# Performance work log

Hardware: AMD Instinct MI355X
Metric: run time of the kernel (lower is better)

The kernel has to match this reference:

```python
import jax, jax.numpy as jnp
import numpy as np

C = 512
H_HEADS = 8  # self-attn heads (num_heads) and cross-attn heads (n_heads), both 8


def _self_attn(x, Wq, Wkv):
    # x: [B,N,C]; shared (ModuleParallel) linear weights, qkv_bias=False
    B, N, _ = x.shape
    h, d = H_HEADS, C // H_HEADS
    q = (x @ Wq.T).reshape(B, N, h, d).transpose(0, 2, 1, 3)          # [B,h,N,d]
    kv = (x @ Wkv.T).reshape(B, N, 2, h, d).transpose(2, 0, 3, 1, 4)  # [2,B,h,N,d]
    k, v = kv[0], kv[1]
    attn = jax.nn.softmax(jnp.einsum('bhnd,bhmd->bhnm', q, k) * (d ** -0.5), axis=-1)
    y = jnp.einsum('bhnm,bhmd->bhnd', attn, v).transpose(0, 2, 1, 3).reshape(B, N, C)
    return y


def _judger(y_self, y_other, Wj1, bj1, Wj2, bj2):
    # Mlp_2(2C->C->C) with exact GELU, then softmax over channel dim
    hdn = jax.nn.gelu(jnp.concatenate([y_self, y_other], axis=-1) @ Wj1.T + bj1, approximate=False)
    return jax.nn.softmax(hdn @ Wj2.T + bj2, axis=-1)


def _cross_attn(yq, ykv, kn_row, vn_row, Win, bin_, Wout, bout, rel):
    # Vectorized form of the per-sample loop: each token is a seq-len-1 query
    # attending over 2 keys: [noise_k + yq, yq * relation_score].
    B, N, _ = yq.shape
    h, d = H_HEADS, C // H_HEADS
    qw, kw, vw = Win[:C], Win[C:2 * C], Win[2 * C:]
    bq, bk, bv = bin_[:C], bin_[C:2 * C], bin_[2 * C:]
    k_in = jnp.stack([kn_row + yq, yq * rel], axis=-2)   # [B,N,2,C]
    v_in = jnp.stack([vn_row + yq, ykv], axis=-2)        # [B,N,2,C]
    qp = (yq @ qw.T + bq).reshape(B, N, h, d)
    kp = (k_in @ kw.T + bk).reshape(B, N, 2, h, d)
    vp = (v_in @ vw.T + bv).reshape(B, N, 2, h, d)
    scores = jnp.einsum('bnhd,bnkhd->bnhk', qp, kp) * (d ** -0.5)
    w = jax.nn.softmax(scores, axis=-1)
    o = jnp.einsum('bnhk,bnkhd->bnhd', w, vp).reshape(B, N, C)
    return o @ Wout.T + bout


def setup_inputs() -> dict:
    key = jax.random.key(0)
    ks = jax.random.split(key, 16)
    B, N = 8, 1024
    s = 0.02
    inp = {
        'x0': jax.random.normal(ks[0], (B, N, C), jnp.float32),
        'x1': jax.random.normal(ks[1], (B, N, C), jnp.float32),
        'H': 32, 'W': 32,
        'Wq': jax.random.normal(ks[2], (C, C), jnp.float32) * s,
        'Wkv': jax.random.normal(ks[3], (2 * C, C), jnp.float32) * s,
        'Wj1': jax.random.normal(ks[4], (C, 2 * C), jnp.float32) * s,
        'bj1': jnp.zeros((C,), jnp.float32),
        'Wj2': jax.random.normal(ks[5], (C, C), jnp.float32) * s,
        'bj2': jnp.zeros((C,), jnp.float32),
        'kn': jax.random.normal(ks[6], (2, C), jnp.float32),
        'vn': jax.random.normal(ks[7], (2, C), jnp.float32),
        'Wc0_in': jax.random.normal(ks[8], (3 * C, C), jnp.float32) * s,
        'bc0_in': jnp.zeros((3 * C,), jnp.float32),
        'Wc0_out': jax.random.normal(ks[9], (C, C), jnp.float32) * s,
        'bc0_out': jnp.zeros((C,), jnp.float32),
        'Wc1_in': jax.random.normal(ks[10], (3 * C, C), jnp.float32) * s,
        'bc1_in': jnp.zeros((3 * C,), jnp.float32),
        'Wc1_out': jax.random.normal(ks[11], (C, C), jnp.float32) * s,
        'bc1_out': jnp.zeros((C,), jnp.float32),
        'Wp': jax.random.normal(ks[12], (C, C), jnp.float32) * s,
        'bp': jnp.zeros((C,), jnp.float32),
    }
    return inp


def reference(x0, x1, H, W, Wq, Wkv, Wj1, bj1, Wj2, bj2, kn, vn,
              Wc0_in, bc0_in, Wc0_out, bc0_out, Wc1_in, bc1_in, Wc1_out, bc1_out,
              Wp, bp):
    # Dual self-attention (shared q/kv projections across modalities, sr_ratio=1)
    y0 = _self_attn(x0, Wq, Wkv)
    y1 = _self_attn(x1, Wq, Wkv)
    # Noise-augmented relation-gated cross-attention (vectorized over batch)
    rel0 = _judger(y0, y1, Wj1, bj1, Wj2, bj2)
    rel1 = _judger(y1, y0, Wj1, bj1, Wj2, bj2)
    new0 = y0 + _cross_attn(y0, y1, kn[0], vn[0], Wc0_in, bc0_in, Wc0_out, bc0_out, rel0)
    new1 = y1 + _cross_attn(y1, y0, kn[1], vn[1], Wc1_in, bc1_in, Wc1_out, bc1_out, rel1)
    out0 = new0 @ Wp.T + bp
    out1 = new1 @ Wp.T + bp
    return jnp.stack([out0, out1])  # [2,B,N,C]
```

## Files before the change

kernel.cpp:

```cpp
#include <hip/hip_runtime.h>

typedef unsigned short u16;
typedef u16 u16x8 __attribute__((ext_vector_type(8)));
typedef __bf16 bf16x8 __attribute__((ext_vector_type(8)));
typedef __bf16 bf16x2 __attribute__((ext_vector_type(2)));
typedef float f32x4 __attribute__((ext_vector_type(4)));

__device__ __forceinline__ float b2f(u16 h) {
  union { unsigned u; float f; } x; x.u = ((unsigned)h) << 16; return x.f;
}
__device__ __forceinline__ u16 f2b(float f) {
  union { float f; unsigned u; } x; x.f = f;
  unsigned r = x.u + 0x7FFFu + ((x.u >> 16) & 1u);
  return (u16)(r >> 16);
}
__device__ __forceinline__ f32x4 mfma16(bf16x8 a, bf16x8 b, f32x4 c) {
  return __builtin_amdgcn_mfma_f32_16x16x32_bf16(a, b, c, 0, 0, 0);
}
__device__ __forceinline__ void gload16(const void* g, void* l) {
  __builtin_amdgcn_global_load_lds(
      (const __attribute__((address_space(1))) void*)g,
      (__attribute__((address_space(3))) void*)l, 16, 0, 0);
}
#define WAITV4 asm volatile("s_waitcnt vmcnt(4)" ::: "memory")
#define WAITV0 asm volatile("s_waitcnt vmcnt(0)" ::: "memory")
#define WAITL0 asm volatile("s_waitcnt lgkmcnt(0)" ::: "memory")
#define BARRIER asm volatile("s_barrier" ::: "memory")

__global__ __launch_bounds__(256) void xcvt_k(const float* __restrict__ x0,
                                              const float* __restrict__ x1,
                                              u16* __restrict__ out) {
  int b = blockIdx.x;
  const float* src = (b < 4096) ? x0 : x1;
  u16* dst = out + (b < 4096 ? 0 : 4194304);
  int i = (b & 4095) * 1024 + threadIdx.x * 4;
  float4 v = *(const float4*)&src[i];
  dst[i + 0] = f2b(v.x); dst[i + 1] = f2b(v.y);
  dst[i + 2] = f2b(v.z); dst[i + 3] = f2b(v.w);
}

__global__ __launch_bounds__(256) void wcvt_k(
    const float* __restrict__ wq, const float* __restrict__ wkv,
    const float* __restrict__ wj1, const float* __restrict__ wj2,
    const float* __restrict__ wci0, const float* __restrict__ wci1,
    const float* __restrict__ wp, u16* __restrict__ wsb) {
  int b = blockIdx.x; const float* src; size_t doff; int lb;
  if      (b < 256)  { src = wq;   doff = 0;       lb = b; }
  else if (b < 768)  { src = wkv;  doff = 262144;  lb = b - 256; }
  else if (b < 1280) { src = wj1;  doff = 786432;  lb = b - 768; }
  else if (b < 1536) { src = wj2;  doff = 1310720; lb = b - 1280; }
  else if (b < 2304) { src = wci0; doff = 1572864; lb = b - 1536; }
  else if (b < 3072) { src = wci1; doff = 2359296; lb = b - 2304; }
  else               { src = wp;   doff = 3145728; lb = b - 3072; }
  int i = lb * 1024 + threadIdx.x * 4;
  float4 v = *(const float4*)&src[i];
  u16* dst = wsb + doff + i;
  u16 c0 = f2b(v.x), c1 = f2b(v.y), c2 = f2b(v.z), c3 = f2b(v.w);
  dst[0] = c0; dst[1] = c1; dst[2] = c2; dst[3] = c3;
  if (b >= 3072) {
    int row = i >> 9, col = i & 511;
    u16* f0 = wsb + 3932160 + (size_t)row * 1024 + col;
    u16* f1 = wsb + 4456448 + (size_t)row * 1024 + col;
    f0[0] = c0; f0[1] = c1; f0[2] = c2; f0[3] = c3;
    f1[0] = c0; f1[1] = c1; f1[2] = c2; f1[3] = c3;
  }
}

__global__ __launch_bounds__(256) void tcvt_k(const float* __restrict__ w0,
                                              const float* __restrict__ w1,
                                              u16* __restrict__ o0,
                                              u16* __restrict__ o1) {
  __shared__ u16 t[64][65];
  const int b = blockIdx.x;
  const float* src = (b & 64) ? w1 : w0;
  u16* dst = (b & 64) ? o1 : o0;
  const int r0 = ((b >> 3) & 7) * 64, c0 = (b & 7) * 64;
  const int tid = threadIdx.x;
#pragma unroll
  for (int i = 0; i < 16; i++) {
    int idx = tid + i * 256;
    int r = idx >> 6, c = idx & 63;
    t[r][c] = f2b(src[(size_t)(r0 + r) * 512 + c0 + c]);
  }
  __syncthreads();
#pragma unroll
  for (int i = 0; i < 16; i++) {
    int idx = tid + i * 256;
    int c = idx >> 6, r = idx & 63;
    dst[(size_t)(c0 + c) * 512 + r0 + r] = t[r][c];
  }
}

__global__ __launch_bounds__(256) void cvec_k(
    const float* __restrict__ kn, const float* __restrict__ vn,
    const float* __restrict__ bp, const float* __restrict__ bco0,
    const float* __restrict__ bco1, const u16* __restrict__ wci0,
    const u16* __restrict__ wci1, const u16* __restrict__ wp,
    float* __restrict__ out) {
  int idx = blockIdx.x * 256 + threadIdx.x;
  int which = idx >> 9, col = idx & 511;
  const float* src; const u16* w; float acc;
  if (which < 4) {
    int s = which & 1, isv = which >> 1;
    src = (isv ? vn : kn) + s * 512;
    w = (s ? wci1 : wci0) + (isv ? 524288 : 262144) + (size_t)col * 512;
    acc = 0.f;
  } else {
    int s = which & 1;
    src = s ? bco1 : bco0;
    w = wp + (size_t)col * 512;
    acc = bp[col];
  }
  for (int k = 0; k < 512; k += 8) {
    u16x8 w8 = *(const u16x8*)&w[k];
#pragma unroll
    for (int j = 0; j < 8; j++) acc += src[k + j] * b2f(w8[j]);
  }
  out[idx] = acc;
}

template<int EPI, int AMODE>
__global__ __launch_bounds__(512, 4) void gemm9_k(
    const u16* __restrict__ A, int astr, int K1, int K,
    const u16* __restrict__ W0, const u16* __restrict__ W1,
    const float* __restrict__ b0, const float* __restrict__ b1,
    void* __restrict__ outp, int ostr, int ncol) {
  __shared__ u16 SM[32768];
  const int tid = threadIdx.x;
  const int lane = tid & 63;
  const int wv = tid >> 6;
  const int wr = wv >> 1, wc = wv & 1;
  const int lr = lane & 15, lg = lane >> 4;
  const int L = blockIdx.x;
  const int nrow = gridDim.x / ncol;
  int row_b, col_b;
  if ((nrow & 7) == 0) {
    int xcd = L & 7, s = L >> 3;
    row_b = xcd * (nrow >> 3) + s / ncol;
    col_b = s % ncol;
  } else { row_b = L % nrow; col_b = L / nrow; }
  const int row0 = row_b * 128, col0 = col_b * 128;
  const int strm = (row0 >= 8192) ? 1 : 0;
  const u16* W = strm ? W1 : W0;
  const float* bias = strm ? b1 : b0;
  const int shift = (AMODE == 4 && col0 >= 1536) ? 512 : 0;
  const int cxor  = (AMODE == 4 && col0 >= 1536) ? 8192 : 0;
  const int rL = tid >> 3;
  const int bcl = (lane & 7) * 16;

  f32x4 acc[2][4];
#pragma unroll
  for (int m = 0; m < 2; m++)
#pragma unroll
    for (int n = 0; n < 4; n++) acc[m][n] = f32x4{0.f, 0.f, 0.f, 0.f};

  const int nk = K >> 6;

  auto stage = [&](int k0, int buf) {
    const int Ab = buf * 16384, Wb = buf * 16384 + 8192;
#pragma unroll
    for (int ch = 0; ch < 2; ch++) {
      int r = ch * 64 + rL;
      int bcs = bcl ^ ((r & 7) << 4);
      const char* asrc;
      if constexpr (AMODE == 3) {
        if (k0 < K1)
          asrc = (const char*)(A + (size_t)(row0 + r) * astr) + k0 * 2 + bcs;
        else
          asrc = (const char*)(A + (size_t)((row0 + r) ^ 8192) * astr) +
                 (k0 - K1) * 2 + bcs;
      } else {
        asrc = (const char*)(A + (size_t)((row0 + r) ^ cxor) * astr) +
               k0 * 2 + bcs;
      }
      gload16(asrc, &SM[Ab + (ch * 64 + wv * 8) * 64]);
      const char* wsrc =
          (const char*)(W + (size_t)(col0 - shift + r) * K) + k0 * 2 + bcs;
      gload16(wsrc, &SM[Wb + (ch * 64 + wv * 8) * 64]);
    }
  };

  stage(0, 0);
  for (int t = 0; t < nk; t++) {
    const int buf = t & 1;
    if (t + 1 < nk) {
      stage((t + 1) * 64, buf ^ 1);
      WAITV4;
    } else {
      WAITV0;
    }
    BARRIER;
    const int Ab = buf * 16384, Wb = buf * 16384 + 8192;
#pragma unroll
    for (int kk = 0; kk < 2; kk++) {
      const int c = kk * 32 + lg * 8;
      bf16x8 af[2], wf[4];
#pragma unroll
      for (int m = 0; m < 2; m++) {
        int r = wr * 32 + m * 16 + lr;
        af[m] = *(const bf16x8*)&SM[Ab + r * 64 + (c ^ ((r & 7) << 3))];
      }
#pragma unroll
      for (int n = 0; n < 4; n++) {
        int r = wc * 64 + n * 16 + lr;
        wf[n] = *(const bf16x8*)&SM[Wb + r * 64 + (c ^ ((r & 7) << 3))];
      }
#pragma unroll
      for (int m = 0; m < 2; m++)
#pragma unroll
        for (int n = 0; n < 4; n++)
          acc[m][n] = mfma16(af[m], wf[n], acc[m][n]);
    }
    WAITL0;
    BARRIER;
  }

#pragma unroll
  for (int m = 0; m < 2; m++)
#pragma unroll
    for (int n = 0; n < 4; n++)
#pragma unroll
      for (int r = 0; r < 4; r++) {
        int grow = row0 + wr * 32 + m * 16 + lg * 4 + r;
        int gcol = col0 + wc * 64 + n * 16 + lr;
        float v = acc[m][n][r];
        if (bias) v += bias[gcol - shift];
        if (EPI == 1) v = 0.5f * v * (1.0f + erff(v * 0.70710678118f));
        if (EPI == 3) ((float*)outp)[(size_t)grow * ostr + gcol] = v;
        else          ((u16*)outp)[(size_t)grow * ostr + gcol] = f2b(v);
      }
}

__global__ __launch_bounds__(256) void vtrans_k(const u16* __restrict__ QKV,
                                                u16* __restrict__ VT) {
  __shared__ u16 t[64][66];
  const int tid = threadIdx.x;
  const int bh = blockIdx.y;
  const int sb = bh >> 3, h = bh & 7;
  const int n0 = blockIdx.x * 64;
#pragma unroll
  for (int i = 0; i < 16; i++) {
    int idx = tid + i * 256;
    int r = idx >> 6, c = idx & 63;
    t[r][c] = QKV[((size_t)sb * 1024 + n0 + r) * 1536 + 1024 + h * 64 + c];
  }
  __syncthreads();
#pragma unroll
  for (int i = 0; i < 16; i++) {
    int idx = tid + i * 256;
    int r = idx >> 6, p = idx & 63;
    int tok = ((p >> 5) << 5) + ((p & 31) >> 1) + ((p & 1) << 4);
    VT[((size_t)bh * 64 + r) * 1024 + n0 + p] = t[tok][r];
  }
}

__global__ __launch_bounds__(256) void attn_k(const u16* __restrict__ QKV,
                                              const u16* __restrict__ VT,
                                              u16* __restrict__ OC) {
  __shared__ u16 Pt[128 * 64];
  const int STR = 1536;
  const int tid = threadIdx.x, lane = tid & 63, wv = tid >> 6;
  const int lr = lane & 15, lg = lane >> 4;
  const int L = blockIdx.x;
  const int by = L & 127;
  const int q0 = (L >> 7) * 128;
  const int sb = by >> 3, h = by & 7;
  const size_t rowbase = (size_t)sb * 1024;
  const float SC = 0.18033688f;

  bf16x8 qa[2][2];
#pragma unroll
  for (int m = 0; m < 2; m++)
#pragma unroll
    for (int kk = 0; kk < 2; kk++) {
      int r = q0 + wv * 32 + m * 16 + lr;
      int c = h * 64 + kk * 32 + lg * 8;
      qa[m][kk] = *(const bf16x8*)&QKV[(rowbase + r) * STR + c];
    }

  f32x4 o[2][4];
#pragma unroll
  for (int m = 0; m < 2; m++)
#pragma unroll
    for (int n = 0; n < 4; n++) o[m][n] = f32x4{0.f, 0.f, 0.f, 0.f};
  float ls[2][4] = {{0.f, 0.f, 0.f, 0.f}, {0.f, 0.f, 0.f, 0.f}};

  for (int t = 0; t < 16; t++) {
    const int c0 = t * 64;
    f32x4 s[2][4];
#pragma unroll
    for (int m = 0; m < 2; m++)
#pragma unroll
      for (int n = 0; n < 4; n++) s[m][n] = f32x4{0.f, 0.f, 0.f, 0.f};
#pragma unroll
    for (int kk = 0; kk < 2; kk++) {
      const int c = kk * 32 + lg * 8;
      bf16x8 kf[4];
#pragma unroll
      for (int n = 0; n < 4; n++) {
        kf[n] = *(const bf16x8*)&QKV[(rowbase + c0 + n * 16 + lr) * STR +
                                     512 + h * 64 + c];
      }
#pragma unroll
      for (int m = 0; m < 2; m++)
#pragma unroll
        for (int n = 0; n < 4; n++) s[m][n] = mfma16(qa[m][kk], kf[n], s[m][n]);
    }
#pragma unroll
    for (int m = 0; m < 2; m++)
#pragma unroll
      for (int r = 0; r < 4; r++) {
        int prow = wv * 32 + m * 16 + lg * 4 + r;
        float p00 = __builtin_amdgcn_exp2f(s[m][0][r] * SC);
        float p01 = __builtin_amdgcn_exp2f(s[m][1][r] * SC);
        float p10 = __builtin_amdgcn_exp2f(s[m][2][r] * SC);
        float p11 = __builtin_amdgcn_exp2f(s[m][3][r] * SC);
        ls[m][r] += (p00 + p01) + (p10 + p11);
        bf16x2 w0; w0[0] = (__bf16)p00; w0[1] = (__bf16)p01;
        bf16x2 w1; w1[0] = (__bf16)p10; w1[1] = (__bf16)p11;
        int ib = prow * 64, xr = (prow & 7) << 3;
        *(bf16x2*)&Pt[ib + ((lr * 2) ^ xr)] = w0;
        *(bf16x2*)&Pt[ib + ((32 + lr * 2) ^ xr)] = w1;
      }
#pragma unroll
    for (int kc = 0; kc < 2; kc++) {
      const int cc = kc * 32 + lg * 8;
      bf16x8 pa[2], vf[4];
#pragma unroll
      for (int m = 0; m < 2; m++) {
        int r = wv * 32 + m * 16 + lr;
        pa[m] = *(const bf16x8*)&Pt[r * 64 + (cc ^ ((r & 7) << 3))];
      }
#pragma unroll
      for (int n = 0; n < 4; n++) {
        vf[n] = *(const bf16x8*)&VT[((size_t)by * 64 + n * 16 + lr) * 1024 +
                                    c0 + cc];
      }
#pragma unroll
      for (int m = 0; m < 2; m++)
#pragma unroll
        for (int n = 0; n < 4; n++) o[m][n] = mfma16(pa[m], vf[n], o[m][n]);
    }
  }

#pragma unroll
  for (int m = 0; m < 2; m++)
#pragma unroll
    for (int r = 0; r < 4; r++) {
      float v = ls[m][r];
      v += __shfl_xor(v, 1); v += __shfl_xor(v, 2);
      v += __shfl_xor(v, 4); v += __shfl_xor(v, 8);
      ls[m][r] = v;
    }
#pragma unroll
  for (int m = 0; m < 2; m++)
#pragma unroll
    for (int n = 0; n < 4; n++)
#pragma unroll
      for (int r = 0; r < 4; r++) {
        int grow = q0 + wv * 32 + m * 16 + lg * 4 + r;
        int gcol = h * 64 + n * 16 + lr;
        OC[(rowbase + grow) * 1024 + gcol] = f2b(o[m][n][r] / ls[m][r]);
      }
}

__global__ __launch_bounds__(256) void relmul_k(const u16* __restrict__ RL,
                                                const u16* __restrict__ OC,
                                                u16* __restrict__ YKR) {
  const int row = blockIdx.x * 4 + (threadIdx.x >> 6);
  const int lane = threadIdx.x & 63;
  u16x8 lv = *(const u16x8*)&RL[(size_t)row * 512 + lane * 8];
  float e[8]; float s = 0.f;
#pragma unroll
  for (int j = 0; j < 8; j++) { e[j] = __expf(b2f(lv[j])); s += e[j]; }
  for (int x = 1; x < 64; x <<= 1) s += __shfl_xor(s, x);
  float inv = 1.0f / s;
  u16x8 y8 = *(const u16x8*)&OC[(size_t)row * 1024 + lane * 8];
  u16x8 o8;
#pragma unroll
  for (int j = 0; j < 8; j++) o8[j] = f2b(b2f(y8[j]) * (e[j] * inv));
  *(u16x8*)&YKR[(size_t)row * 512 + lane * 8] = o8;
}

__global__ __launch_bounds__(256) void twokey3_k(const u16* __restrict__ CP,
                                                 const u16* __restrict__ KP1,
                                                 const float* __restrict__ cvec,
                                                 u16* __restrict__ OC) {
  const int t = blockIdx.x * 4 + (threadIdx.x >> 6);
  const int lane = threadIdx.x & 63;
  const int s = t >> 13;
  const size_t rb = (size_t)t * 2048 + lane * 8;
  u16x8 q8 = *(const u16x8*)&CP[rb];
  u16x8 a8 = *(const u16x8*)&CP[rb + 512];
  u16x8 v0 = *(const u16x8*)&CP[rb + 1024];
  u16x8 v1 = *(const u16x8*)&CP[rb + 1536];
  u16x8 b8 = *(const u16x8*)&KP1[(size_t)t * 512 + lane * 8];
  const float* ck = cvec + s * 512 + lane * 8;
  const float* cv = cvec + 1024 + s * 512 + lane * 8;

  float s0 = 0.f, s1 = 0.f;
#pragma unroll
  for (int j = 0; j < 8; j++) {
    float qf = b2f(q8[j]);
    s0 += qf * (b2f(a8[j]) + ck[j]);
    s1 += qf * b2f(b8[j]);
  }
  s0 += __shfl_xor(s0, 1); s1 += __shfl_xor(s1, 1);
  s0 += __shfl_xor(s0, 2); s1 += __shfl_xor(s1, 2);
  s0 += __shfl_xor(s0, 4); s1 += __shfl_xor(s1, 4);

  float e0 = __expf(s0 * 0.125f), e1 = __expf(s1 * 0.125f);
  float rr = 1.0f / (e0 + e1);
  float w0 = e0 * rr, w1 = e1 * rr;
  u16x8 o8;
#pragma unroll
  for (int j = 0; j < 8; j++)
    o8[j] = f2b(w0 * (b2f(v0[j]) + cv[j]) + w1 * b2f(v1[j]));
  *(u16x8*)&OC[(size_t)t * 1024 + 512 + lane * 8] = o8;
}

extern "C" void kernel_launch(void* const* d_in, const int* in_sizes, int n_in,
                              void* d_out, int out_size, void* d_ws, size_t ws_size,
                              hipStream_t stream) {
  (void)in_sizes; (void)n_in; (void)out_size; (void)ws_size;
  const float* x0  = (const float*)d_in[0];
  const float* x1  = (const float*)d_in[1];
  const float* Wq  = (const float*)d_in[4];
  const float* Wkv = (const float*)d_in[5];
  const float* Wj1 = (const float*)d_in[6];
  const float* bj1 = (const float*)d_in[7];
  const float* Wj2 = (const float*)d_in[8];
  const float* bj2 = (const float*)d_in[9];
  const float* kn  = (const float*)d_in[10];
  const float* vn  = (const float*)d_in[11];
  const float* Wci[2]  = {(const float*)d_in[12], (const float*)d_in[16]};
  const float* bci[2]  = {(const float*)d_in[13], (const float*)d_in[17]};
  const float* Wco[2]  = {(const float*)d_in[14], (const float*)d_in[18]};
  const float* bco[2]  = {(const float*)d_in[15], (const float*)d_in[19]};
  const float* Wp  = (const float*)d_in[20];
  const float* bp  = (const float*)d_in[21];

  u16* wsb = (u16*)d_ws;
  u16* wqb   = wsb;
  u16* wj1b  = wsb + 786432;
  u16* wj2b  = wsb + 1310720;
  u16* wcib[2] = {wsb + 1572864, wsb + 2359296};
  u16* wpb   = wsb + 3145728;
  u16* wcoT[2] = {wsb + 3407872, wsb + 3670016};
  u16* wfin[2] = {wsb + 3932160, wsb + 4456448};
  float* cvecb = (float*)(wsb + 4980736);
  const size_t SLOT = 8388608;
  u16* base = wsb + 5242880;
  u16* S0 = base;
  u16* OC = base + 1 * SLOT;
  u16* S3 = base + 3 * SLOT;
  u16* S4 = base + 4 * SLOT;
  u16* S6 = base + 6 * SLOT;
  u16* QKV = S3;
  u16* REL = S3;
  u16* CP  = S3;
  u16* YKR = S4;

  dim3 blk(256), gblk(512);
  xcvt_k<<<dim3(8192), blk, 0, stream>>>(x0, x1, S0);
  wcvt_k<<<dim3(3328), blk, 0, stream>>>(Wq, Wkv, Wj1, Wj2, Wci[0], Wci[1],
                                         Wp, wsb);
  tcvt_k<<<dim3(128), blk, 0, stream>>>(Wco[0], Wco[1], wcoT[0], wcoT[1]);
  cvec_k<<<dim3(12), blk, 0, stream>>>(kn, vn, bp, bco[0], bco[1],
                                       wcib[0], wcib[1], wpb, cvecb);
  for (int s = 0; s < 2; s++)
    gemm9_k<0, 0><<<dim3(16), gblk, 0, stream>>>(
        wpb, 512, 512, 512, wcoT[s], wcoT[s], nullptr, nullptr,
        wfin[s] + 512, 1024, 4);

  gemm9_k<0, 0><<<dim3(1536), gblk, 0, stream>>>(
      S0, 512, 512, 512, wqb, wqb, nullptr, nullptr, QKV, 1536, 12);
  vtrans_k<<<dim3(16, 128), blk, 0, stream>>>(QKV, S6);
  attn_k<<<dim3(1024), blk, 0, stream>>>(QKV, S6, OC);

  gemm9_k<1, 3><<<dim3(512), gblk, 0, stream>>>(
      OC, 1024, 512, 1024, wj1b, wj1b, bj1, bj1, S0, 512, 4);
  gemm9_k<0, 0><<<dim3(512), gblk, 0, stream>>>(
      S0, 512, 512, 512, wj2b, wj2b, bj2, bj2, REL, 512, 4);
  relmul_k<<<dim3(4096), blk, 0, stream>>>(REL, OC, YKR);
  gemm9_k<0, 0><<<dim3(512), gblk, 0, stream>>>(
      YKR, 512, 512, 512, wcib[0] + 262144, wcib[1] + 262144,
      bci[0] + 512, bci[1] + 512, S0, 512, 4);
  gemm9_k<0, 4><<<dim3(2048), gblk, 0, stream>>>(
      OC, 1024, 512, 512, wcib[0], wcib[1], bci[0], bci[1], CP, 2048, 16);

  twokey3_k<<<dim3(4096), blk, 0, stream>>>(CP, S0, cvecb, OC);

  gemm9_k<3, 0><<<dim3(512), gblk, 0, stream>>>(
      OC, 1024, 1024, 1024, wfin[0], wfin[1], cvecb + 2048, cvecb + 2560,
      d_out, 512, 4);
}
```

Measured before the change: 384.2 us.

## Double-buffer K/V tiles in LDS via async global_load_lds in attention kernel

```diff
diff --git a/kernel.cpp b/kernel.cpp
--- a/kernel.cpp
+++ b/kernel.cpp
@@ -257,7 +257,7 @@
 __global__ __launch_bounds__(256) void attn_k(const u16* __restrict__ QKV,
                                               const u16* __restrict__ VT,
                                               u16* __restrict__ OC) {
-  __shared__ u16 Pt[128 * 64];
+  __shared__ u16 SM[24576];
   const int STR = 1536;
   const int tid = threadIdx.x, lane = tid & 63, wv = tid >> 6;
   const int lr = lane & 15, lg = lane >> 4;
@@ -266,6 +266,7 @@
   const int q0 = (L >> 7) * 128;
   const int sb = by >> 3, h = by & 7;
   const size_t rowbase = (size_t)sb * 1024;
+  const int bcl = (lane & 7) * 16;
   const float SC = 0.18033688f;
 
   bf16x8 qa[2][2];
@@ -285,27 +286,53 @@
     for (int n = 0; n < 4; n++) o[m][n] = f32x4{0.f, 0.f, 0.f, 0.f};
   float ls[2][4] = {{0.f, 0.f, 0.f, 0.f}, {0.f, 0.f, 0.f, 0.f}};
 
+  auto stagekv = [&](int c0, int buf) {
+#pragma unroll
+    for (int ch = 0; ch < 2; ch++) {
+      int r = ch * 32 + (tid >> 3);
+      int bcs = bcl ^ ((r & 7) << 4);
+      const char* ks =
+          (const char*)(QKV + (rowbase + c0 + r) * STR + 512 + h * 64) + bcs;
+      gload16(ks, &SM[buf * 8192 + (ch * 32 + wv * 8) * 64]);
+      const char* vs =
+          (const char*)(VT + ((size_t)by * 64 + r) * 1024 + c0) + bcs;
+      gload16(vs, &SM[buf * 8192 + 4096 + (ch * 32 + wv * 8) * 64]);
+    }
+  };
+
+  stagekv(0, 0);
   for (int t = 0; t < 16; t++) {
-    const int c0 = t * 64;
+    const int buf = t & 1;
+    if (t < 15) {
+      stagekv((t + 1) * 64, buf ^ 1);
+      WAITV4;
+    } else {
+      WAITV0;
+    }
+    BARRIER;
+    const int Kb = buf * 8192, Vb = buf * 8192 + 4096;
+
     f32x4 s[2][4];
 #pragma unroll
     for (int m = 0; m < 2; m++)
 #pragma unroll
       for (int n = 0; n < 4; n++) s[m][n] = f32x4{0.f, 0.f, 0.f, 0.f};
+    __builtin_amdgcn_s_setprio(1);
 #pragma unroll
     for (int kk = 0; kk < 2; kk++) {
       const int c = kk * 32 + lg * 8;
       bf16x8 kf[4];
 #pragma unroll
       for (int n = 0; n < 4; n++) {
-        kf[n] = *(const bf16x8*)&QKV[(rowbase + c0 + n * 16 + lr) * STR +
-                                     512 + h * 64 + c];
+        int r = n * 16 + lr;
+        kf[n] = *(const bf16x8*)&SM[Kb + r * 64 + (c ^ ((r & 7) << 3))];
       }
 #pragma unroll
       for (int m = 0; m < 2; m++)
 #pragma unroll
         for (int n = 0; n < 4; n++) s[m][n] = mfma16(qa[m][kk], kf[n], s[m][n]);
     }
+    __builtin_amdgcn_s_setprio(0);
 #pragma unroll
     for (int m = 0; m < 2; m++)
 #pragma unroll
@@ -318,10 +345,11 @@
         ls[m][r] += (p00 + p01) + (p10 + p11);
         bf16x2 w0; w0[0] = (__bf16)p00; w0[1] = (__bf16)p01;
         bf16x2 w1; w1[0] = (__bf16)p10; w1[1] = (__bf16)p11;
-        int ib = prow * 64, xr = (prow & 7) << 3;
-        *(bf16x2*)&Pt[ib + ((lr * 2) ^ xr)] = w0;
-        *(bf16x2*)&Pt[ib + ((32 + lr * 2) ^ xr)] = w1;
-      }
+        int ib = 16384 + prow * 64, xr = (prow & 7) << 3;
+        *(bf16x2*)&SM[ib + ((lr * 2) ^ xr)] = w0;
+        *(bf16x2*)&SM[ib + ((32 + lr * 2) ^ xr)] = w1;
+      }
+    __builtin_amdgcn_s_setprio(1);
 #pragma unroll
     for (int kc = 0; kc < 2; kc++) {
       const int cc = kc * 32 + lg * 8;
@@ -329,18 +357,21 @@
 #pragma unroll
       for (int m = 0; m < 2; m++) {
         int r = wv * 32 + m * 16 + lr;
-        pa[m] = *(const bf16x8*)&Pt[r * 64 + (cc ^ ((r & 7) << 3))];
+        pa[m] = *(const bf16x8*)&SM[16384 + r * 64 + (cc ^ ((r & 7) << 3))];
       }
 #pragma unroll
       for (int n = 0; n < 4; n++) {
-        vf[n] = *(const bf16x8*)&VT[((size_t)by * 64 + n * 16 + lr) * 1024 +
-                                    c0 + cc];
+        int r = n * 16 + lr;
+        vf[n] = *(const bf16x8*)&SM[Vb + r * 64 + (cc ^ ((r & 7) << 3))];
       }
 #pragma unroll
       for (int m = 0; m < 2; m++)
 #pragma unroll
         for (int n = 0; n < 4; n++) o[m][n] = mfma16(pa[m], vf[n], o[m][n]);
     }
+    __builtin_amdgcn_s_setprio(0);
+    WAITL0;
+    BARRIER;
   }
 
 #pragma unroll
```

New measurement: 321.0 us. 16.5% less time.
